# Optimization experiments

Hardware: AMD Instinct MI355X
Metric: run time of the kernel (lower is better)

The kernel has to match this reference:

```python
import jax, jax.numpy as jnp
import numpy as np

DIM = 768
NUM_HEADS = 12
HEAD_DIM = DIM // NUM_HEADS
SCALE = HEAD_DIM ** -0.5


def setup_inputs() -> dict:
    key = jax.random.key(0)
    ks = jax.random.split(key, 7)
    B, N, C = 8, 1024, DIM
    x = jax.random.normal(ks[0], (B, N, C), dtype=jnp.float32)
    mask = jax.random.randint(ks[1], (B, N), 0, 2) > 0  # True = masked out
    qkv_w = jax.random.normal(ks[2], (3 * C, C), dtype=jnp.float32) * 0.02
    q_bias = jax.random.normal(ks[3], (C,), dtype=jnp.float32) * 0.02
    v_bias = jax.random.normal(ks[4], (C,), dtype=jnp.float32) * 0.02
    proj_w = jax.random.normal(ks[5], (C, C), dtype=jnp.float32) * 0.02
    proj_b = jax.random.normal(ks[6], (C,), dtype=jnp.float32) * 0.02
    return {"x": x, "mask": mask, "qkv_w": qkv_w, "q_bias": q_bias,
            "v_bias": v_bias, "proj_w": proj_w, "proj_b": proj_b}


def reference(x, mask, qkv_w, q_bias, v_bias, proj_w, proj_b):
    B, N, C = x.shape
    # CAE bias: concat(q_bias, zeros, v_bias) for the fused qkv projection
    qkv_bias = jnp.concatenate([q_bias, jnp.zeros_like(v_bias), v_bias])
    qkv = x @ qkv_w.T + qkv_bias  # [B, N, 3C]
    qkv = qkv.reshape(B, N, 3, NUM_HEADS, HEAD_DIM)
    q, k, v = (qkv[:, :, i].transpose(0, 2, 1, 3) for i in range(3))  # [B,H,N,hd]
    attn = jnp.einsum('bhqd,bhkd->bhqk', q * SCALE, k)  # [B,H,N,N]
    attn = jnp.where(mask[:, None, None, :], -jnp.inf, attn)
    attn = jax.nn.softmax(attn, axis=-1)
    out = jnp.einsum('bhqk,bhkd->bhqd', attn, v)  # [B,H,N,hd]
    out = out.transpose(0, 2, 1, 3).reshape(B, N, C)
    return out @ proj_w.T + proj_b
```

## Files before the change

### kernel.cpp

```cpp
#include <hip/hip_runtime.h>
#include <cstddef>
#include <cstdint>


typedef __attribute__((ext_vector_type(4))) float f32x4;
typedef __attribute__((ext_vector_type(8))) __bf16 bf16x8;
typedef __attribute__((ext_vector_type(4))) unsigned int uint4v;
typedef __attribute__((ext_vector_type(2))) unsigned int uint2v;

#define QK_PRESCALE 0.18033688011112042f

__device__ __forceinline__ unsigned short f2bf(float f) {
  return (unsigned short)((__float_as_uint(f) + 0x8000u) >> 16);
}
__device__ __forceinline__ unsigned int pack2bf(float flo, float fhi) {
  unsigned ulo = __float_as_uint(flo) + 0x8000u;
  unsigned uhi = __float_as_uint(fhi) + 0x8000u;
  return __builtin_amdgcn_perm(uhi, ulo, 0x07060302);
}

__device__ __forceinline__ void gl_lds16(const unsigned short* g, unsigned short* l) {
  __builtin_amdgcn_global_load_lds(
      (const __attribute__((address_space(1))) unsigned int*)g,
      (__attribute__((address_space(3))) unsigned int*)l, 16, 0, 0);
}

__global__ __launch_bounds__(256)
void cvt3_kernel(const float* __restrict__ s0, unsigned short* __restrict__ d0,
                 const float* __restrict__ s1, unsigned short* __restrict__ d1,
                 const float* __restrict__ s2, unsigned short* __restrict__ d2) {
  int bid = blockIdx.x;
  const float* s; unsigned short* d; int i; int n4;
  if (bid < 6144)      { s = s0; d = d0; i = bid * 256 + threadIdx.x;            n4 = 1572864; }
  else if (bid < 7872) { s = s1; d = d1; i = (bid - 6144) * 256 + threadIdx.x;   n4 = 442368; }
  else                 { s = s2; d = d2; i = (bid - 7872) * 256 + threadIdx.x;   n4 = 147456; }
  if (i < n4) {
    float4 v = ((const float4*)s)[i];
    uint2v o;
    o.x = pack2bf(v.x, v.y);
    o.y = pack2bf(v.z, v.w);
    ((uint2v*)d)[i] = o;
  }
}

__device__ __forceinline__ int a0row(int o) { return (o < 10) ? o * 8 : 144 + (o - 10) * 8; }
__device__ __forceinline__ int a1row(int o) { return (o < 8) ? 80 + o * 8 : 224 + (o - 8) * 8; }

__global__ __launch_bounds__(512, 2)
void qkv_gemm(const unsigned short* __restrict__ xb, const unsigned short* __restrict__ wb,
              const float* __restrict__ qb, const float* __restrict__ vb,
              unsigned short* __restrict__ qo, unsigned short* __restrict__ ko,
              unsigned short* __restrict__ vto) {
  __shared__ __align__(16) unsigned short lds[69632];
  const int tid = threadIdx.x;
  const int lane = tid & 63, wid = tid >> 6;
  const int widu = __builtin_amdgcn_readfirstlane(wid);
  const int lm = lane & 15, lq = lane >> 4;
  const int xsw = lm & 7;
  const int wr = widu >> 2, wc = widu & 3;
  const int L = blockIdx.x;
  const int xcd = L & 7, s = L >> 3;
  const int tt = xcd * 4 + (s >> 3);
  const int ft = s & 7;
  const int m0 = tt * 256;
  const int n0 = ft * 288;
  const int srow = lane >> 3;
  const int scolsw = ((lane & 7) ^ srow) * 8;
  const unsigned short* paS = wb + (size_t)(n0 + srow) * 768 + scolsw;
  const unsigned short* pbS = xb + (size_t)(m0 + srow) * 768 + scolsw;

  const int a0n3 = (widu < 4);
  const int a0o = a0n3 ? widu * 3 : 12 + (widu - 4) * 2;
  const int a0r0 = a0row(a0o), a0r1 = a0row(a0o + 1);
  const int a0r2 = a0n3 ? a0row(a0o + 2) : 0;
  const int a1r0 = a1row(2 * widu), a1r1 = a1row(2 * widu + 1);
  const int b0q0 = (2 * widu) >> 2, b0q1 = (2 * widu + 1) >> 2;
  const int b0r0 = b0q0 * 64 + ((2 * widu) & 3) * 8;
  const int b0r1 = b0q1 * 64 + ((2 * widu + 1) & 3) * 8;
  const int b1r0 = b0r0 + 32, b1r1 = b0r1 + 32;

  f32x4 acc[9][4] = {};

#define STAGE_A0(tgt) { const size_t _c = (size_t)(tgt) * 64; const int _b = ((tgt) & 1) * 18432; \
    gl_lds16(paS + (size_t)a0r0 * 768 + _c, &lds[_b + a0r0 * 64]); \
    gl_lds16(paS + (size_t)a0r1 * 768 + _c, &lds[_b + a0r1 * 64]); \
    if (a0n3) gl_lds16(paS + (size_t)a0r2 * 768 + _c, &lds[_b + a0r2 * 64]); }

#define STAGE_A1(tgt) { const size_t _c = (size_t)(tgt) * 64; const int _b = ((tgt) & 1) * 18432; \
    gl_lds16(paS + (size_t)a1r0 * 768 + _c, &lds[_b + a1r0 * 64]); \
    gl_lds16(paS + (size_t)a1r1 * 768 + _c, &lds[_b + a1r1 * 64]); }

#define STAGE_B0(tgt) { const size_t _c = (size_t)(tgt) * 64; const int _b = 36864 + ((tgt) & 1) * 16384; \
    gl_lds16(pbS + (size_t)b0r0 * 768 + _c, &lds[_b + b0r0 * 64]); \
    gl_lds16(pbS + (size_t)b0r1 * 768 + _c, &lds[_b + b0r1 * 64]); }

#define STAGE_B1(tgt) { const size_t _c = (size_t)(tgt) * 64; const int _b = 36864 + ((tgt) & 1) * 16384; \
    gl_lds16(pbS + (size_t)b1r0 * 768 + _c, &lds[_b + b1r0 * 64]); \
    gl_lds16(pbS + (size_t)b1r1 * 768 + _c, &lds[_b + b1r1 * 64]); }

#define WAIT_G() { if (a0n3) asm volatile("s_waitcnt vmcnt(5)" ::: "memory"); \
                   else      asm volatile("s_waitcnt vmcnt(4)" ::: "memory"); \
                   asm volatile("s_barrier" ::: "memory"); }
#define BAR_E()   asm volatile("s_waitcnt lgkmcnt(0)\ns_barrier" ::: "memory")

  STAGE_A0(0); STAGE_B0(0); STAGE_A1(0); STAGE_B1(0);
  STAGE_A0(1); STAGE_B0(1);
  WAIT_G();

  for (int t = 0; t < 12; ++t) {
    const int b = t & 1;
    const int tn1 = (t + 1 < 12) ? t + 1 : 11;
    const int tn2 = (t + 2 < 12) ? t + 2 : 11;
    const unsigned short* Ab = &lds[b * 18432];
    const unsigned short* Bb = &lds[36864 + b * 16384];

    bf16x8 bff[4][2], af[5][2];
#pragma unroll
    for (int n2 = 0; n2 < 4; ++n2)
#pragma unroll
      for (int kx = 0; kx < 2; ++kx)
        bff[n2][kx] = *(const bf16x8*)&Bb[(wc * 64 + n2 * 16 + lm) * 64 + (((kx * 4 + lq) ^ xsw) * 8)];
#pragma unroll
    for (int m2 = 0; m2 < 5; ++m2)
#pragma unroll
      for (int kx = 0; kx < 2; ++kx)
        af[m2][kx] = *(const bf16x8*)&Ab[(wr * 144 + m2 * 16 + lm) * 64 + (((kx * 4 + lq) ^ xsw) * 8)];

    STAGE_A1(tn1); STAGE_B1(tn1);

    __builtin_amdgcn_s_setprio(1);
#pragma unroll
    for (int kx = 0; kx < 2; ++kx)
#pragma unroll
      for (int m2 = 0; m2 < 5; ++m2)
#pragma unroll
        for (int n2 = 0; n2 < 4; ++n2)
          acc[m2][n2] = __builtin_amdgcn_mfma_f32_16x16x32_bf16(af[m2][kx], bff[n2][kx], acc[m2][n2], 0, 0, 0);
    __builtin_amdgcn_s_setprio(0);

    bf16x8 af2[4][2];
#pragma unroll
    for (int m2 = 0; m2 < 4; ++m2)
#pragma unroll
      for (int kx = 0; kx < 2; ++kx)
        af2[m2][kx] = *(const bf16x8*)&Ab[(wr * 144 + (5 + m2) * 16 + lm) * 64 + (((kx * 4 + lq) ^ xsw) * 8)];
    __builtin_amdgcn_s_setprio(1);
#pragma unroll
    for (int kx = 0; kx < 2; ++kx)
#pragma unroll
      for (int m2 = 0; m2 < 4; ++m2)
#pragma unroll
        for (int n2 = 0; n2 < 4; ++n2)
          acc[5 + m2][n2] = __builtin_amdgcn_mfma_f32_16x16x32_bf16(af2[m2][kx], bff[n2][kx], acc[5 + m2][n2], 0, 0, 0);
    __builtin_amdgcn_s_setprio(0);

    BAR_E();
    STAGE_A0(tn2); STAGE_B0(tn2);
    WAIT_G();
  }
  asm volatile("s_waitcnt vmcnt(0)" ::: "memory");

#undef STAGE_A0
#undef STAGE_A1
#undef STAGE_B0
#undef STAGE_B1

  const int bq = tt >> 2;
  const int tokb = (tt & 3) * 256;
#pragma unroll
  for (int mi = 0; mi < 9; ++mi) {
    const int fblk = n0 + wr * 144 + mi * 16;
    if (fblk < 1536) {
      const bool isq = fblk < 768;
      unsigned short* dst0 = isq ? qo : ko;
      const int fd = fblk - (isq ? 0 : 768);
      const int hh = fd >> 6;
      const int dih = (fd & 63) + lq * 4;
      f32x4 bias4 = {0.f, 0.f, 0.f, 0.f};
      if (isq) bias4 = *(const f32x4*)&qb[fblk + lq * 4];
#pragma unroll
      for (int ni = 0; ni < 4; ++ni) {
        const int tok = tokb + wc * 64 + ni * 16 + lm;
        uint2v pk;
        if (isq) {
          pk.x = pack2bf((acc[mi][ni][0] + bias4[0]) * QK_PRESCALE,
                         (acc[mi][ni][1] + bias4[1]) * QK_PRESCALE);
          pk.y = pack2bf((acc[mi][ni][2] + bias4[2]) * QK_PRESCALE,
                         (acc[mi][ni][3] + bias4[3]) * QK_PRESCALE);
        } else {
          pk.x = pack2bf(acc[mi][ni][0], acc[mi][ni][1]);
          pk.y = pack2bf(acc[mi][ni][2], acc[mi][ni][3]);
        }
        *(uint2v*)&dst0[(((size_t)(bq * 12 + hh)) * 1024 + tok) * 64 + dih] = pk;
      }
    }
  }
  if (n0 + 288 > 1536) {
#pragma unroll
    for (int p = 0; p < 2; ++p) {
      __syncthreads();
      if (wr == p) {
#pragma unroll
        for (int mi = 0; mi < 9; ++mi) {
          const int fblk = n0 + p * 144 + mi * 16;
          if (fblk >= 1536) {
            f32x4 bias4 = *(const f32x4*)&vb[fblk - 1536 + lq * 4];
#pragma unroll
            for (int ni = 0; ni < 4; ++ni) {
              const int tokl = wc * 64 + ni * 16 + lm;
#pragma unroll
              for (int r = 0; r < 4; ++r)
                lds[(mi * 16 + lq * 4 + r) * 264 + tokl] = f2bf(acc[mi][ni][r] + bias4[r]);
            }
          }
        }
      }
      __syncthreads();
      const int fv = 1536 - (n0 + p * 144);
      const int rv0 = fv > 0 ? fv : 0;
      for (int r = rv0 + (tid >> 2); r < 144; r += 128) {
        const int tq = tid & 3;
        const int dgv = n0 + p * 144 + r - 1536;
        const int hh = dgv >> 6, d = dgv & 63;
        unsigned short* dstv = vto + (((size_t)(bq * 12 + hh)) * 64 + d) * 1024 + tokb + tq * 64;
        const unsigned short* srcr = &lds[r * 264 + tq * 64];
#pragma unroll
        for (int j = 0; j < 8; ++j)
          *(uint4v*)&dstv[j * 8] = *(const uint4v*)&srcr[j * 8];
      }
    }
  }
}

__global__ __launch_bounds__(256, 3)
void attn_mfma(const unsigned short* __restrict__ q, const unsigned short* __restrict__ k,
               const unsigned short* __restrict__ vt, const int* __restrict__ mask,
               unsigned short* __restrict__ ao) {
  __shared__ unsigned short ks_s[2][64 * 64];
  __shared__ unsigned short vs_s[2][64 * 64];
  __shared__ unsigned short ps[4][32 * 40];
  __shared__ float mkl[1024];
  const int tid = threadIdx.x;
  const int lane = tid & 63, wid = tid >> 6;
  const int lm = lane & 15, lq = lane >> 4;
  const int xsw = lm & 7;
  const int sxor = (lm & 8) >> 1;
  const int L = blockIdx.x;
  const int xcd = L & 7, s = L >> 3;
  const int bh = xcd * 12 + s / 8;
  const int qt = s % 8;
  const int bb = bh / 12, hh = bh % 12;
  const unsigned short* qp = q + (size_t)bh * 65536;
  const unsigned short* kp = k + (size_t)bh * 65536;
  const unsigned short* vp = vt + (size_t)bh * 65536;
  const int* mp = mask + bb * 1024;
  const int q0 = qt * 128 + wid * 32;
  const int srow = lane >> 3;
  const int scolsw = ((lane & 7) ^ srow) * 8;
  const unsigned short* gk = kp + (size_t)(wid * 16 + srow) * 64 + scolsw;
  const unsigned short* gv = vp + (size_t)(wid * 16 + srow) * 1024 + scolsw;

#define STAGE_T(kt_, b_) { \
    gl_lds16(gk + (size_t)(kt_) * 4096, &ks_s[b_][(wid * 16) * 64]); \
    gl_lds16(gk + (size_t)(kt_) * 4096 + (size_t)8 * 64, &ks_s[b_][(wid * 16 + 8) * 64]); \
    gl_lds16(gv + (size_t)(kt_) * 64, &vs_s[b_][(wid * 16) * 64]); \
    gl_lds16(gv + (size_t)(kt_) * 64 + (size_t)8 * 1024, &vs_s[b_][(wid * 16 + 8) * 64]); }

  {
    int4 mv = ((const int4*)mp)[tid];
    float4 f;
    f.x = mv.x ? -1e30f : 0.0f;
    f.y = mv.y ? -1e30f : 0.0f;
    f.z = mv.z ? -1e30f : 0.0f;
    f.w = mv.w ? -1e30f : 0.0f;
    ((float4*)mkl)[tid] = f;
  }

  bf16x8 qf[2][2];
#pragma unroll
  for (int mi = 0; mi < 2; ++mi)
#pragma unroll
    for (int ks2 = 0; ks2 < 2; ++ks2)
      qf[mi][ks2] = *(const bf16x8*)&qp[(size_t)(q0 + mi * 16 + lm) * 64 + ks2 * 32 + lq * 8];
  bf16x8 ones;
#pragma unroll
  for (int i = 0; i < 8; ++i) ones[i] = (__bf16)1.0f;

  f32x4 o_acc[2][4] = {};
  f32x4 l_acc[2] = {};

  STAGE_T(0, 0);
  __syncthreads();

  for (int kt = 0; kt < 16; ++kt) {
    const int b = kt & 1;
    if (kt) {
      asm volatile("s_waitcnt vmcnt(0)\ns_barrier" ::: "memory");
    }
    if (kt < 15) STAGE_T(kt + 1, b ^ 1);

    f32x4 st[4][2] = {};
#pragma unroll
    for (int ks2 = 0; ks2 < 2; ++ks2) {
      bf16x8 kf[4];
#pragma unroll
      for (int nt = 0; nt < 4; ++nt)
        kf[nt] = *(const bf16x8*)&ks_s[b][(nt * 16 + lm) * 64 + (((ks2 * 4 + lq) ^ xsw) * 8)];
      __builtin_amdgcn_s_setprio(1);
#pragma unroll
      for (int nt = 0; nt < 4; ++nt)
#pragma unroll
        for (int mi = 0; mi < 2; ++mi)
          st[nt][mi] = __builtin_amdgcn_mfma_f32_16x16x32_bf16(kf[nt], qf[mi][ks2], st[nt][mi], 0, 0, 0);
      __builtin_amdgcn_s_setprio(0);
    }

#pragma unroll
    for (int h2 = 0; h2 < 2; ++h2) {
#pragma unroll
      for (int ntl = 0; ntl < 2; ++ntl) {
        const int nt = h2 * 2 + ntl;
        f32x4 mv4 = *(const f32x4*)&mkl[kt * 64 + nt * 16 + lq * 4];
#pragma unroll
        for (int mi = 0; mi < 2; ++mi) {
          uint2v pk;
          pk.x = pack2bf(__builtin_amdgcn_exp2f(st[nt][mi][0] + mv4[0]),
                         __builtin_amdgcn_exp2f(st[nt][mi][1] + mv4[1]));
          pk.y = pack2bf(__builtin_amdgcn_exp2f(st[nt][mi][2] + mv4[2]),
                         __builtin_amdgcn_exp2f(st[nt][mi][3] + mv4[3]));
          *(uint2v*)&ps[wid][(mi * 16 + lm) * 40 + ((ntl * 16 + lq * 4) ^ sxor)] = pk;
        }
      }
      bf16x8 pf[2], vf[4];
#pragma unroll
      for (int mi = 0; mi < 2; ++mi) {
        uint2v h0 = *(const uint2v*)&ps[wid][(mi * 16 + lm) * 40 + ((lq * 8) ^ sxor)];
        uint2v h1 = *(const uint2v*)&ps[wid][(mi * 16 + lm) * 40 + ((lq * 8 + 4) ^ sxor)];
        uint4v u; u.x = h0.x; u.y = h0.y; u.z = h1.x; u.w = h1.y;
        pf[mi] = __builtin_bit_cast(bf16x8, u);
      }
#pragma unroll
      for (int nt = 0; nt < 4; ++nt)
        vf[nt] = *(const bf16x8*)&vs_s[b][(nt * 16 + lm) * 64 + (((h2 * 4 + lq) ^ xsw) * 8)];
      __builtin_amdgcn_s_setprio(1);
#pragma unroll
      for (int mi = 0; mi < 2; ++mi) {
#pragma unroll
        for (int nt = 0; nt < 4; ++nt)
          o_acc[mi][nt] = __builtin_amdgcn_mfma_f32_16x16x32_bf16(pf[mi], vf[nt], o_acc[mi][nt], 0, 0, 0);
        l_acc[mi] = __builtin_amdgcn_mfma_f32_16x16x32_bf16(pf[mi], ones, l_acc[mi], 0, 0, 0);
      }
      __builtin_amdgcn_s_setprio(0);
    }
  }
#undef STAGE_T

#pragma unroll
  for (int mi = 0; mi < 2; ++mi) {
#pragma unroll
    for (int r = 0; r < 4; ++r) {
      float inv = 1.0f / l_acc[mi][r];
      int tok = q0 + mi * 16 + lq * 4 + r;
#pragma unroll
      for (int nt = 0; nt < 4; ++nt)
        ao[(size_t)(bb * 1024 + tok) * 768 + hh * 64 + nt * 16 + lm] = f2bf(o_acc[mi][nt][r] * inv);
    }
  }
}

__global__ __launch_bounds__(256)
void proj_gemm(const unsigned short* __restrict__ ab, const unsigned short* __restrict__ wb,
               const float* __restrict__ pb, float* __restrict__ out) {
  __shared__ unsigned short as[128 * 64];
  __shared__ unsigned short bs[128 * 64];
  const int tid = threadIdx.x;
  const int lane = tid & 63, wid = tid >> 6;
  const int lm = lane & 15, lq = lane >> 4;
  const int xsw = lm & 7;
  const int wm = (wid & 1) * 64, wn = (wid >> 1) * 64;
  const int L = blockIdx.x;
  const int xcd = L & 7, s = L >> 3;
  const int m0 = (xcd * 8 + s / 6) * 128;
  const int n0 = (s % 6) * 128;
  const int srow = lane >> 3;
  const int scolsw = ((lane & 7) ^ srow) * 8;
  const unsigned short* ga = wb + (size_t)(n0 + wid * 32 + srow) * 768 + scolsw;
  const unsigned short* gb = ab + (size_t)(m0 + wid * 32 + srow) * 768 + scolsw;
  f32x4 acc[4][4] = {};
  for (int kt = 0; kt < 768; kt += 64) {
#pragma unroll
    for (int i = 0; i < 4; ++i) {
      gl_lds16(ga + kt + (size_t)i * 8 * 768, &as[(wid * 32 + i * 8) * 64]);
      gl_lds16(gb + kt + (size_t)i * 8 * 768, &bs[(wid * 32 + i * 8) * 64]);
    }
    __syncthreads();
#pragma unroll
    for (int ks = 0; ks < 2; ++ks) {
      bf16x8 af[4], bf[4];
#pragma unroll
      for (int i = 0; i < 4; ++i)
        af[i] = *(const bf16x8*)&as[(wm + i * 16 + lm) * 64 + (((ks * 4 + lq) ^ xsw) * 8)];
#pragma unroll
      for (int i = 0; i < 4; ++i)
        bf[i] = *(const bf16x8*)&bs[(wn + i * 16 + lm) * 64 + (((ks * 4 + lq) ^ xsw) * 8)];
#pragma unroll
      for (int mi = 0; mi < 4; ++mi)
#pragma unroll
        for (int ni = 0; ni < 4; ++ni)
          acc[mi][ni] = __builtin_amdgcn_mfma_f32_16x16x32_bf16(af[mi], bf[ni], acc[mi][ni], 0, 0, 0);
    }
    __syncthreads();
  }
#pragma unroll
  for (int mi = 0; mi < 4; ++mi) {
    int gn0 = n0 + wm + mi * 16 + lq * 4;
    f32x4 bias4 = *(const f32x4*)&pb[gn0];
#pragma unroll
    for (int ni = 0; ni < 4; ++ni) {
      int gm = m0 + wn + ni * 16 + lm;
      f32x4 o;
      o[0] = acc[mi][ni][0] + bias4[0];
      o[1] = acc[mi][ni][1] + bias4[1];
      o[2] = acc[mi][ni][2] + bias4[2];
      o[3] = acc[mi][ni][3] + bias4[3];
      *(f32x4*)&out[(size_t)gm * 768 + gn0] = o;
    }
  }
}

extern "C" void kernel_launch(void* const* d_in, const int* in_sizes, int n_in,
                              void* d_out, int out_size, void* d_ws, size_t ws_size,
                              hipStream_t stream) {
  const float* x      = (const float*)d_in[0];
  const int*   mask   = (const int*)d_in[1];
  const float* qkv_w  = (const float*)d_in[2];
  const float* q_bias = (const float*)d_in[3];
  const float* v_bias = (const float*)d_in[4];
  const float* proj_w = (const float*)d_in[5];
  const float* proj_b = (const float*)d_in[6];
  float* out = (float*)d_out;
  unsigned short* p = (unsigned short*)d_ws;
  unsigned short* xb     = p;              p += 6291456;
  unsigned short* wqkvb  = p;              p += 1769472;
  unsigned short* wprojb = p;              p += 589824;
  unsigned short* qo     = p;              p += 6291456;
  unsigned short* ko     = p;              p += 6291456;
  unsigned short* vto    = p;              p += 6291456;
  unsigned short* ao     = p;

  cvt3_kernel<<<8448, 256, 0, stream>>>(x, xb, qkv_w, wqkvb, proj_w, wprojb);
  qkv_gemm<<<256, 512, 0, stream>>>(xb, wqkvb, q_bias, v_bias, qo, ko, vto);
  attn_mfma<<<768, 256, 0, stream>>>(qo, ko, vto, mask, ao);
  proj_gemm<<<384, 256, 0, stream>>>(ao, wprojb, proj_b, out);
}
```

Before: 182.1 us.

## Shrink QKV GEMM tile to 288x128 with 4 waves and drop software pipelining

The QKV projection GEMM moves from 512-thread blocks computing 288x256 tiles with a double-buffered, hand-scheduled async LDS pipeline to 256-thread blocks computing 288x128 tiles with a single LDS buffer and a simple load/sync/compute/sync loop. The grid doubles to 512 blocks and LDS per block drops sharply, so more blocks can be resident per CU. The intent is to gain occupancy and simpler scheduling in place of explicit prefetch overlap. The cost is exposed global-load latency each K step and lower reuse of the weight tile per block.

```diff
diff --git a/kernel.cpp b/kernel.cpp
--- a/kernel.cpp
+++ b/kernel.cpp
@@ -43,90 +43,54 @@
   }
 }
 
-__device__ __forceinline__ int a0row(int o) { return (o < 10) ? o * 8 : 144 + (o - 10) * 8; }
-__device__ __forceinline__ int a1row(int o) { return (o < 8) ? 80 + o * 8 : 224 + (o - 8) * 8; }
-
-__global__ __launch_bounds__(512, 2)
+__global__ __launch_bounds__(256, 2)
 void qkv_gemm(const unsigned short* __restrict__ xb, const unsigned short* __restrict__ wb,
               const float* __restrict__ qb, const float* __restrict__ vb,
               unsigned short* __restrict__ qo, unsigned short* __restrict__ ko,
               unsigned short* __restrict__ vto) {
-  __shared__ __align__(16) unsigned short lds[69632];
+  __shared__ __align__(16) unsigned short lds[26624];
   const int tid = threadIdx.x;
   const int lane = tid & 63, wid = tid >> 6;
   const int widu = __builtin_amdgcn_readfirstlane(wid);
   const int lm = lane & 15, lq = lane >> 4;
   const int xsw = lm & 7;
-  const int wr = widu >> 2, wc = widu & 3;
+  const int wr = widu >> 1, wc = widu & 1;
   const int L = blockIdx.x;
   const int xcd = L & 7, s = L >> 3;
-  const int tt = xcd * 4 + (s >> 3);
+  const int tt = xcd * 8 + (s >> 3);
   const int ft = s & 7;
-  const int m0 = tt * 256;
+  const int m0 = tt * 128;
   const int n0 = ft * 288;
   const int srow = lane >> 3;
   const int scolsw = ((lane & 7) ^ srow) * 8;
-  const unsigned short* paS = wb + (size_t)(n0 + srow) * 768 + scolsw;
-  const unsigned short* pbS = xb + (size_t)(m0 + srow) * 768 + scolsw;
-
-  const int a0n3 = (widu < 4);
-  const int a0o = a0n3 ? widu * 3 : 12 + (widu - 4) * 2;
-  const int a0r0 = a0row(a0o), a0r1 = a0row(a0o + 1);
-  const int a0r2 = a0n3 ? a0row(a0o + 2) : 0;
-  const int a1r0 = a1row(2 * widu), a1r1 = a1row(2 * widu + 1);
-  const int b0q0 = (2 * widu) >> 2, b0q1 = (2 * widu + 1) >> 2;
-  const int b0r0 = b0q0 * 64 + ((2 * widu) & 3) * 8;
-  const int b0r1 = b0q1 * 64 + ((2 * widu + 1) & 3) * 8;
-  const int b1r0 = b0r0 + 32, b1r1 = b0r1 + 32;
+  const unsigned short* paS = wb + (size_t)(n0 + widu * 72 + srow) * 768 + scolsw;
+  const unsigned short* pbS = xb + (size_t)(m0 + widu * 32 + srow) * 768 + scolsw;
+  unsigned short* const ldsA = &lds[(widu * 72) * 64];
+  unsigned short* const ldsB = &lds[18432 + (widu * 32) * 64];
 
   f32x4 acc[9][4] = {};
 
-#define STAGE_A0(tgt) { const size_t _c = (size_t)(tgt) * 64; const int _b = ((tgt) & 1) * 18432; \
-    gl_lds16(paS + (size_t)a0r0 * 768 + _c, &lds[_b + a0r0 * 64]); \
-    gl_lds16(paS + (size_t)a0r1 * 768 + _c, &lds[_b + a0r1 * 64]); \
-    if (a0n3) gl_lds16(paS + (size_t)a0r2 * 768 + _c, &lds[_b + a0r2 * 64]); }
-
-#define STAGE_A1(tgt) { const size_t _c = (size_t)(tgt) * 64; const int _b = ((tgt) & 1) * 18432; \
-    gl_lds16(paS + (size_t)a1r0 * 768 + _c, &lds[_b + a1r0 * 64]); \
-    gl_lds16(paS + (size_t)a1r1 * 768 + _c, &lds[_b + a1r1 * 64]); }
-
-#define STAGE_B0(tgt) { const size_t _c = (size_t)(tgt) * 64; const int _b = 36864 + ((tgt) & 1) * 16384; \
-    gl_lds16(pbS + (size_t)b0r0 * 768 + _c, &lds[_b + b0r0 * 64]); \
-    gl_lds16(pbS + (size_t)b0r1 * 768 + _c, &lds[_b + b0r1 * 64]); }
-
-#define STAGE_B1(tgt) { const size_t _c = (size_t)(tgt) * 64; const int _b = 36864 + ((tgt) & 1) * 16384; \
-    gl_lds16(pbS + (size_t)b1r0 * 768 + _c, &lds[_b + b1r0 * 64]); \
-    gl_lds16(pbS + (size_t)b1r1 * 768 + _c, &lds[_b + b1r1 * 64]); }
-
-#define WAIT_G() { if (a0n3) asm volatile("s_waitcnt vmcnt(5)" ::: "memory"); \
-                   else      asm volatile("s_waitcnt vmcnt(4)" ::: "memory"); \
-                   asm volatile("s_barrier" ::: "memory"); }
-#define BAR_E()   asm volatile("s_waitcnt lgkmcnt(0)\ns_barrier" ::: "memory")
-
-  STAGE_A0(0); STAGE_B0(0); STAGE_A1(0); STAGE_B1(0);
-  STAGE_A0(1); STAGE_B0(1);
-  WAIT_G();
-
   for (int t = 0; t < 12; ++t) {
-    const int b = t & 1;
-    const int tn1 = (t + 1 < 12) ? t + 1 : 11;
-    const int tn2 = (t + 2 < 12) ? t + 2 : 11;
-    const unsigned short* Ab = &lds[b * 18432];
-    const unsigned short* Bb = &lds[36864 + b * 16384];
+    const size_t c = (size_t)t * 64;
+#pragma unroll
+    for (int i = 0; i < 9; ++i)
+      gl_lds16(paS + (size_t)i * 8 * 768 + c, ldsA + i * 8 * 64);
+#pragma unroll
+    for (int i = 0; i < 4; ++i)
+      gl_lds16(pbS + (size_t)i * 8 * 768 + c, ldsB + i * 8 * 64);
+    __syncthreads();
 
     bf16x8 bff[4][2], af[5][2];
 #pragma unroll
     for (int n2 = 0; n2 < 4; ++n2)
 #pragma unroll
       for (int kx = 0; kx < 2; ++kx)
-        bff[n2][kx] = *(const bf16x8*)&Bb[(wc * 64 + n2 * 16 + lm) * 64 + (((kx * 4 + lq) ^ xsw) * 8)];
+        bff[n2][kx] = *(const bf16x8*)&lds[18432 + (wc * 64 + n2 * 16 + lm) * 64 + (((kx * 4 + lq) ^ xsw) * 8)];
 #pragma unroll
     for (int m2 = 0; m2 < 5; ++m2)
 #pragma unroll
       for (int kx = 0; kx < 2; ++kx)
-        af[m2][kx] = *(const bf16x8*)&Ab[(wr * 144 + m2 * 16 + lm) * 64 + (((kx * 4 + lq) ^ xsw) * 8)];
-
-    STAGE_A1(tn1); STAGE_B1(tn1);
+        af[m2][kx] = *(const bf16x8*)&lds[(wr * 144 + m2 * 16 + lm) * 64 + (((kx * 4 + lq) ^ xsw) * 8)];
 
     __builtin_amdgcn_s_setprio(1);
 #pragma unroll
@@ -143,7 +107,7 @@
     for (int m2 = 0; m2 < 4; ++m2)
 #pragma unroll
       for (int kx = 0; kx < 2; ++kx)
-        af2[m2][kx] = *(const bf16x8*)&Ab[(wr * 144 + (5 + m2) * 16 + lm) * 64 + (((kx * 4 + lq) ^ xsw) * 8)];
+        af2[m2][kx] = *(const bf16x8*)&lds[(wr * 144 + (5 + m2) * 16 + lm) * 64 + (((kx * 4 + lq) ^ xsw) * 8)];
     __builtin_amdgcn_s_setprio(1);
 #pragma unroll
     for (int kx = 0; kx < 2; ++kx)
@@ -154,19 +118,11 @@
           acc[5 + m2][n2] = __builtin_amdgcn_mfma_f32_16x16x32_bf16(af2[m2][kx], bff[n2][kx], acc[5 + m2][n2], 0, 0, 0);
     __builtin_amdgcn_s_setprio(0);
 
-    BAR_E();
-    STAGE_A0(tn2); STAGE_B0(tn2);
-    WAIT_G();
-  }
-  asm volatile("s_waitcnt vmcnt(0)" ::: "memory");
-
-#undef STAGE_A0
-#undef STAGE_A1
-#undef STAGE_B0
-#undef STAGE_B1
-
-  const int bq = tt >> 2;
-  const int tokb = (tt & 3) * 256;
+    __syncthreads();
+  }
+
+  const int bq = tt >> 3;
+  const int tokb = (tt & 7) * 128;
 #pragma unroll
   for (int mi = 0; mi < 9; ++mi) {
     const int fblk = n0 + wr * 144 + mi * 16;
@@ -210,7 +166,7 @@
               const int tokl = wc * 64 + ni * 16 + lm;
 #pragma unroll
               for (int r = 0; r < 4; ++r)
-                lds[(mi * 16 + lq * 4 + r) * 264 + tokl] = f2bf(acc[mi][ni][r] + bias4[r]);
+                lds[(mi * 16 + lq * 4 + r) * 136 + tokl] = f2bf(acc[mi][ni][r] + bias4[r]);
             }
           }
         }
@@ -218,12 +174,12 @@
       __syncthreads();
       const int fv = 1536 - (n0 + p * 144);
       const int rv0 = fv > 0 ? fv : 0;
-      for (int r = rv0 + (tid >> 2); r < 144; r += 128) {
-        const int tq = tid & 3;
+      for (int r = rv0 + (tid >> 1); r < 144; r += 128) {
+        const int tq = tid & 1;
         const int dgv = n0 + p * 144 + r - 1536;
         const int hh = dgv >> 6, d = dgv & 63;
         unsigned short* dstv = vto + (((size_t)(bq * 12 + hh)) * 64 + d) * 1024 + tokb + tq * 64;
-        const unsigned short* srcr = &lds[r * 264 + tq * 64];
+        const unsigned short* srcr = &lds[r * 136 + tq * 64];
 #pragma unroll
         for (int j = 0; j < 8; ++j)
           *(uint4v*)&dstv[j * 8] = *(const uint4v*)&srcr[j * 8];
@@ -449,7 +405,7 @@
   unsigned short* ao     = p;
 
   cvt3_kernel<<<8448, 256, 0, stream>>>(x, xb, qkv_w, wqkvb, proj_w, wprojb);
-  qkv_gemm<<<256, 512, 0, stream>>>(xb, wqkvb, q_bias, v_bias, qo, ko, vto);
+  qkv_gemm<<<512, 256, 0, stream>>>(xb, wqkvb, q_bias, v_bias, qo, ko, vto);
   attn_mfma<<<768, 256, 0, stream>>>(qo, ko, vto, mask, ao);
   proj_gemm<<<384, 256, 0, stream>>>(ao, wprojb, proj_b, out);
 }
```

New measurement: 182.7 us. No clear change (+0.3%).
